# Kernel tuning notes

Hardware: AMD Instinct MI355X
Metric: run time of the kernel (lower is better)

Reference implementation:

```python
import jax, jax.numpy as jnp
import numpy as np

B, S, D = 8, 1024, 256


def _linear_params(key, d):
    k1, k2 = jax.random.split(key)
    lim = 1.0 / np.sqrt(d)
    W = jax.random.uniform(k1, (d, d), jnp.float32, -lim, lim)
    b = jax.random.uniform(k2, (d,), jnp.float32, -lim, lim)
    return W, b


def setup_inputs() -> dict:
    key = jax.random.key(0)
    ks = jax.random.split(key, 7)
    x = jax.random.normal(ks[0], (B, S, D), jnp.float32)
    Wq, bq = _linear_params(ks[1], D)
    Wk, bk = _linear_params(ks[2], D)
    Wv, bv = _linear_params(ks[3], D)
    Wf, bf = _linear_params(ks[4], D)
    Wi, bi = _linear_params(ks[5], D)
    Wo, bo = _linear_params(ks[6], D)
    return {"x": x, "Wq": Wq, "bq": bq, "Wk": Wk, "bk": bk, "Wv": Wv, "bv": bv,
            "Wf": Wf, "bf": bf, "Wi": Wi, "bi": bi, "Wo": Wo, "bo": bo}


def reference(x, Wq, bq, Wk, bk, Wv, bv, Wf, bf, Wi, bi, Wo, bo):
    # Projections (torch Linear stores W as [out, in])
    q = x @ Wq.T + bq
    k = x @ Wk.T + bk
    v = x @ Wq.T + bq  # faithful to source: forward uses self.W_q(x) for v (W_v unused)
    f = jax.nn.sigmoid(x @ Wf.T + bf)  # forget gate, sigmoid
    i = jnp.exp(x @ Wi.T + bi)         # input gate, exp

    # time-major xs: each (S, B, D)
    xs = tuple(jnp.swapaxes(a, 0, 1) for a in (f, i, k, v, q))
    C0 = jnp.zeros((x.shape[0], x.shape[2], x.shape[2]), x.dtype)  # matrix memory [B,D,D]
    n0 = jnp.zeros((x.shape[0], x.shape[2]), x.dtype)              # normalizer [B,D]

    def step(carry, t):
        C, n = carry
        ft, it, kt, vt, qt = t
        # C_t = f_t * C_{t-1} + i_t * v_t k_t^T  (gates broadcast over key dim)
        C = ft[:, :, None] * C + it[:, :, None] * (vt[:, :, None] * kt[:, None, :])
        n = ft * n + it * kt
        num = jnp.einsum('bik,bk->bi', C, qt)
        den = jnp.maximum(jnp.abs(jnp.einsum('bk,bk->b', n, qt)), 1.0)[:, None]
        return (C, n), num / den

    _, h = jax.lax.scan(step, (C0, n0), xs)
    h = jnp.swapaxes(h, 0, 1)  # (B, S, D)
    return h @ Wo.T + bo
```

## Files before the change

### kernel.cpp

```cpp
#include <hip/hip_runtime.h>
#include <math.h>

namespace {

constexpr int Bn = 8;
constexpr int Sn = 1024;
constexpr int Dn = 256;
constexpr int Mn = Bn * Sn;
constexpr int L  = 32;
constexpr int NSEG = Sn / L;

typedef __attribute__((ext_vector_type(8))) short short8;
typedef __attribute__((ext_vector_type(4))) float f32x4;

__device__ float g_den[Bn * Sn];

__device__ __forceinline__ float sigmoidf_(float x) {
    return 1.0f / (1.0f + __expf(-x));
}

__device__ __forceinline__ unsigned short f2bf(float x) {
    unsigned int u = __float_as_uint(x);
    return (unsigned short)((u + 0x7FFF + ((u >> 16) & 1)) >> 16);
}
__device__ __forceinline__ float bf2f(unsigned short h) {
    return __uint_as_float(((unsigned int)h) << 16);
}

__global__ __launch_bounds__(256) void split_xw(
    const float* __restrict__ X,
    const float* __restrict__ Wq, const float* __restrict__ Wk,
    const float* __restrict__ Wf, const float* __restrict__ Wi,
    unsigned short* __restrict__ Xh, unsigned short* __restrict__ Xl,
    unsigned short* __restrict__ Wh, unsigned short* __restrict__ Wl)
{
    const int i = blockIdx.x * 256 + threadIdx.x;
    const float4* src;
    unsigned short* dh;
    unsigned short* dl;
    size_t off;
    if (i < 524288) {
        src = (const float4*)X + i;
        dh = Xh; dl = Xl;
        off = (size_t)i * 4;
    } else {
        const int j = i - 524288;
        const int w = j >> 14;
        const int r = j & 16383;
        const float* Wp = (w == 0) ? Wq : (w == 1) ? Wk : (w == 2) ? Wf : Wi;
        src = (const float4*)Wp + r;
        dh = Wh; dl = Wl;
        off = ((size_t)w << 16) + (size_t)r * 4;
    }
    const float4 v = *src;
    ushort4 h, l;
    h.x = f2bf(v.x); l.x = f2bf(v.x - bf2f(h.x));
    h.y = f2bf(v.y); l.y = f2bf(v.y - bf2f(h.y));
    h.z = f2bf(v.z); l.z = f2bf(v.z - bf2f(h.z));
    h.w = f2bf(v.w); l.w = f2bf(v.w - bf2f(h.w));
    *(ushort4*)(dh + off) = h;
    *(ushort4*)(dl + off) = l;
}

__global__ __launch_bounds__(256) void split_pn(
    const float* __restrict__ Pn, const float* __restrict__ Wo,
    unsigned short* __restrict__ Ph, unsigned short* __restrict__ Pl,
    unsigned short* __restrict__ Woh, unsigned short* __restrict__ Wol)
{
    const int i = blockIdx.x * 256 + threadIdx.x;
    float4 v;
    unsigned short* dh;
    unsigned short* dl;
    size_t off;
    if (i < 524288) {
        const float invd = 1.0f / fmaxf(fabsf(g_den[i >> 6]), 1.0f);
        v = ((const float4*)Pn)[i];
        v.x *= invd; v.y *= invd; v.z *= invd; v.w *= invd;
        dh = Ph; dl = Pl;
        off = (size_t)i * 4;
    } else {
        const int j = i - 524288;
        v = ((const float4*)Wo)[j];
        dh = Woh; dl = Wol;
        off = (size_t)j * 4;
    }
    ushort4 h, l;
    h.x = f2bf(v.x); l.x = f2bf(v.x - bf2f(h.x));
    h.y = f2bf(v.y); l.y = f2bf(v.y - bf2f(h.y));
    h.z = f2bf(v.z); l.z = f2bf(v.z - bf2f(h.z));
    h.w = f2bf(v.w); l.w = f2bf(v.w - bf2f(h.w));
    *(ushort4*)(dh + off) = h;
    *(ushort4*)(dl + off) = l;
}

__global__ __launch_bounds__(256) void proj_gemm2(
    const unsigned short* __restrict__ Xh, const unsigned short* __restrict__ Xl,
    const unsigned short* __restrict__ Wh, const unsigned short* __restrict__ Wl,
    const float* __restrict__ b0, const float* __restrict__ b1,
    const float* __restrict__ b2, const float* __restrict__ b3,
    float* __restrict__ Y0, float* __restrict__ Y1,
    float* __restrict__ Y2, float* __restrict__ Y3)
{
    __shared__ unsigned short Ahs[128][40];
    __shared__ unsigned short Als[128][40];
    __shared__ unsigned short Bhs[128][40];
    __shared__ unsigned short Bls[128][40];

    const int tid = threadIdx.x;
    const int mb  = blockIdx.x * 128;
    const int nbg = blockIdx.y;
    const int widx = nbg >> 1;
    const int ro   = (nbg & 1) * 128;

    const float* bsel = (widx == 0) ? b0 : (widx == 1) ? b1 : (widx == 2) ? b2 : b3;
    float*       Ysel = (widx == 0) ? Y0 : (widx == 1) ? Y1 : (widx == 2) ? Y2 : Y3;

    const int lane = tid & 63;
    const int wv   = tid >> 6;
    const int wm   = (wv >> 1) * 64;
    const int wn   = (wv & 1) * 64;
    const int quad = lane >> 4;
    const int l16  = lane & 15;
    const int srow = tid >> 1;
    const int skq  = (tid & 1) * 16;

    const size_t abase = (size_t)(mb + srow) * Dn + skq;
    const size_t bbase = (size_t)(nbg * 128 + srow) * Dn + skq;

    f32x4 acc[4][4];
    #pragma unroll
    for (int mt = 0; mt < 4; ++mt)
        #pragma unroll
        for (int nt = 0; nt < 4; ++nt)
            acc[mt][nt] = (f32x4){0.f, 0.f, 0.f, 0.f};

    short8 pah0, pah1, pal0, pal1, pbh0, pbh1, pbl0, pbl1;
    pah0 = *(const short8*)(Xh + abase);     pah1 = *(const short8*)(Xh + abase + 8);
    pal0 = *(const short8*)(Xl + abase);     pal1 = *(const short8*)(Xl + abase + 8);
    pbh0 = *(const short8*)(Wh + bbase);     pbh1 = *(const short8*)(Wh + bbase + 8);
    pbl0 = *(const short8*)(Wl + bbase);     pbl1 = *(const short8*)(Wl + bbase + 8);

    for (int k0 = 0; k0 < Dn; k0 += 32) {
        __syncthreads();
        *(short8*)&Ahs[srow][skq]     = pah0;
        *(short8*)&Ahs[srow][skq + 8] = pah1;
        *(short8*)&Als[srow][skq]     = pal0;
        *(short8*)&Als[srow][skq + 8] = pal1;
        *(short8*)&Bhs[srow][skq]     = pbh0;
        *(short8*)&Bhs[srow][skq + 8] = pbh1;
        *(short8*)&Bls[srow][skq]     = pbl0;
        *(short8*)&Bls[srow][skq + 8] = pbl1;
        __syncthreads();

        if (k0 + 32 < Dn) {
            const size_t ka = abase + k0 + 32;
            const size_t kb = bbase + k0 + 32;
            pah0 = *(const short8*)(Xh + ka); pah1 = *(const short8*)(Xh + ka + 8);
            pal0 = *(const short8*)(Xl + ka); pal1 = *(const short8*)(Xl + ka + 8);
            pbh0 = *(const short8*)(Wh + kb); pbh1 = *(const short8*)(Wh + kb + 8);
            pbl0 = *(const short8*)(Wl + kb); pbl1 = *(const short8*)(Wl + kb + 8);
        }

        short8 afh[4], afl[4];
        #pragma unroll
        for (int mt = 0; mt < 4; ++mt) {
            const int row = wm + mt * 16 + l16;
            afh[mt] = *(const short8*)&Ahs[row][quad * 8];
            afl[mt] = *(const short8*)&Als[row][quad * 8];
        }
        #pragma unroll
        for (int nt = 0; nt < 4; ++nt) {
            const int row = wn + nt * 16 + l16;
            const short8 bfh = *(const short8*)&Bhs[row][quad * 8];
            const short8 bfl = *(const short8*)&Bls[row][quad * 8];
            #pragma unroll
            for (int mt = 0; mt < 4; ++mt) {
                acc[mt][nt] = __builtin_amdgcn_mfma_f32_16x16x32_bf16(
                    afh[mt], bfh, acc[mt][nt], 0, 0, 0);
                acc[mt][nt] = __builtin_amdgcn_mfma_f32_16x16x32_bf16(
                    afh[mt], bfl, acc[mt][nt], 0, 0, 0);
                acc[mt][nt] = __builtin_amdgcn_mfma_f32_16x16x32_bf16(
                    afl[mt], bfh, acc[mt][nt], 0, 0, 0);
            }
        }
    }

    #pragma unroll
    for (int nt = 0; nt < 4; ++nt) {
        const int col = ro + wn + nt * 16 + l16;
        const float bv = bsel[col];
        #pragma unroll
        for (int mt = 0; mt < 4; ++mt) {
            const int rowb = mb + wm + mt * 16 + quad * 4;
            #pragma unroll
            for (int r = 0; r < 4; ++r) {
                float v = acc[mt][nt][r] + bv;
                if (widx == 2)      v = sigmoidf_(v);
                else if (widx == 3) v = __expf(v);
                Ysel[(size_t)(rowb + r) * Dn + col] = v;
            }
        }
    }
}

__global__ __launch_bounds__(256) void out_gemm2(
    const unsigned short* __restrict__ Ph, const unsigned short* __restrict__ Pl,
    const unsigned short* __restrict__ Woh, const unsigned short* __restrict__ Wol,
    const float* __restrict__ bias, float* __restrict__ Y)
{
    __shared__ unsigned short Ahs[64][40];
    __shared__ unsigned short Als[64][40];
    __shared__ unsigned short Bhs[64][40];
    __shared__ unsigned short Bls[64][40];

    const int tid = threadIdx.x;
    const int mb  = blockIdx.x * 64;
    const int nb  = blockIdx.y * 64;

    const int lane = tid & 63;
    const int wv   = tid >> 6;
    const int wm   = (wv >> 1) * 32;
    const int wn   = (wv & 1) * 32;
    const int quad = lane >> 4;
    const int l16  = lane & 15;
    const int srow = tid >> 2;
    const int skq  = (tid & 3) * 8;

    const size_t abase = (size_t)(mb + srow) * Dn + skq;
    const size_t bbase = (size_t)(nb + srow) * Dn + skq;

    f32x4 acc[2][2];
    #pragma unroll
    for (int mt = 0; mt < 2; ++mt)
        #pragma unroll
        for (int nt = 0; nt < 2; ++nt)
            acc[mt][nt] = (f32x4){0.f, 0.f, 0.f, 0.f};

    short8 pah, pal, pbh, pbl;
    pah = *(const short8*)(Ph  + abase);
    pal = *(const short8*)(Pl  + abase);
    pbh = *(const short8*)(Woh + bbase);
    pbl = *(const short8*)(Wol + bbase);

    for (int k0 = 0; k0 < Dn; k0 += 32) {
        __syncthreads();
        *(short8*)&Ahs[srow][skq] = pah;
        *(short8*)&Als[srow][skq] = pal;
        *(short8*)&Bhs[srow][skq] = pbh;
        *(short8*)&Bls[srow][skq] = pbl;
        __syncthreads();

        if (k0 + 32 < Dn) {
            const size_t ka = abase + k0 + 32;
            const size_t kb = bbase + k0 + 32;
            pah = *(const short8*)(Ph  + ka);
            pal = *(const short8*)(Pl  + ka);
            pbh = *(const short8*)(Woh + kb);
            pbl = *(const short8*)(Wol + kb);
        }

        short8 afh[2], afl[2];
        #pragma unroll
        for (int mt = 0; mt < 2; ++mt) {
            const int row = wm + mt * 16 + l16;
            afh[mt] = *(const short8*)&Ahs[row][quad * 8];
            afl[mt] = *(const short8*)&Als[row][quad * 8];
        }
        #pragma unroll
        for (int nt = 0; nt < 2; ++nt) {
            const int row = wn + nt * 16 + l16;
            const short8 bfh = *(const short8*)&Bhs[row][quad * 8];
            const short8 bfl = *(const short8*)&Bls[row][quad * 8];
            #pragma unroll
            for (int mt = 0; mt < 2; ++mt) {
                acc[mt][nt] = __builtin_amdgcn_mfma_f32_16x16x32_bf16(
                    afh[mt], bfh, acc[mt][nt], 0, 0, 0);
                acc[mt][nt] = __builtin_amdgcn_mfma_f32_16x16x32_bf16(
                    afh[mt], bfl, acc[mt][nt], 0, 0, 0);
                acc[mt][nt] = __builtin_amdgcn_mfma_f32_16x16x32_bf16(
                    afl[mt], bfh, acc[mt][nt], 0, 0, 0);
            }
        }
    }

    #pragma unroll
    for (int nt = 0; nt < 2; ++nt) {
        const int col = nb + wn + nt * 16 + l16;
        const float bv = bias[col];
        #pragma unroll
        for (int mt = 0; mt < 2; ++mt) {
            const int rowb = mb + wm + mt * 16 + quad * 4;
            #pragma unroll
            for (int r = 0; r < 4; ++r) {
                Y[(size_t)(rowb + r) * Dn + col] = acc[mt][nt][r] + bv;
            }
        }
    }
}

__global__ __launch_bounds__(256) void prep(
    const float* __restrict__ Pf, const float* __restrict__ Pi,
    const float* __restrict__ Pk, const float* __restrict__ Pq,
    float* __restrict__ Gc, float* __restrict__ Vt, float* __restrict__ Nt,
    float* __restrict__ Aend, float* __restrict__ un, float* __restrict__ Ssm)
{
    const int m = blockIdx.x;
    const int b = blockIdx.y;
    const int tid = threadIdx.x;

    if (tid < L) g_den[b * Sn + m * L + tid] = 0.0f;

    {
        const int r = tid;
        const size_t base = (size_t)b * Sn * Dn + (size_t)m * L * Dn + r;
        float G = 1.0f, Nacc = 0.0f;
        #pragma unroll 4
        for (int t = 0; t < L; ++t) {
            const size_t off = base + (size_t)t * Dn;
            const float f  = Pf[off];
            const float iv = Pi[off];
            const float kv = Pk[off];
            const float vv = Pq[off];
            G *= f;
            const float rG = 1.0f / G;
            Gc[off] = G;
            Vt[off] = iv * vv * rG;
            Nacc = fmaf(iv * kv, rG, Nacc);
            Nt[off] = Nacc;
        }
        const size_t s = ((size_t)b * NSEG + m) * Dn + r;
        Aend[s] = G;
        un[s]   = G * Nacc;
    }

    {
        const size_t qb = (size_t)b * Sn * Dn + (size_t)m * L * Dn;
        const int tau = tid >> 3;
        const int s4  = (tid & 7) * 4;

        float a0 = 0.f, a1 = 0.f, a2 = 0.f, a3 = 0.f;
        #pragma unroll 4
        for (int c = 0; c < Dn; c += 4) {
            const float4 q4 = *(const float4*)(Pq + qb + (size_t)tau * Dn + c);
            const float4 k0 = *(const float4*)(Pk + qb + (size_t)(s4 + 0) * Dn + c);
            const float4 k1 = *(const float4*)(Pk + qb + (size_t)(s4 + 1) * Dn + c);
            const float4 k2 = *(const float4*)(Pk + qb + (size_t)(s4 + 2) * Dn + c);
            const float4 k3 = *(const float4*)(Pk + qb + (size_t)(s4 + 3) * Dn + c);
            a0 += q4.x*k0.x + q4.y*k0.y + q4.z*k0.z + q4.w*k0.w;
            a1 += q4.x*k1.x + q4.y*k1.y + q4.z*k1.z + q4.w*k1.w;
            a2 += q4.x*k2.x + q4.y*k2.y + q4.z*k2.z + q4.w*k2.w;
            a3 += q4.x*k3.x + q4.y*k3.y + q4.z*k3.z + q4.w*k3.w;
        }
        float* outp = Ssm + ((size_t)b * NSEG + m) * L * L + (size_t)tau * L + s4;
        outp[0] = (s4 + 0 <= tau) ? a0 : 0.0f;
        outp[1] = (s4 + 1 <= tau) ? a1 : 0.0f;
        outp[2] = (s4 + 2 <= tau) ? a2 : 0.0f;
        outp[3] = (s4 + 3 <= tau) ? a3 : 0.0f;
    }
}

__global__ __launch_bounds__(256) void ut_gemm(
    const float* __restrict__ Pk, const float* __restrict__ Vt,
    const float* __restrict__ Aend, float* __restrict__ UT)
{
    __shared__ float As[L][68];
    __shared__ float Bs[L][68];

    const int bm   = blockIdx.x;
    const int tile = blockIdx.y;
    const int cb   = (tile >> 2) * 64;
    const int rb   = (tile & 3) * 64;
    const int b    = bm >> 5;
    const int m    = bm & 31;
    const size_t kb = (size_t)b * Sn * Dn + (size_t)m * L * Dn;
    const int tid = threadIdx.x;

    #pragma unroll
    for (int n = 0; n < 8; ++n) {
        const int e  = n * 256 + tid;
        const int sg = e >> 6;
        const int cc = e & 63;
        As[sg][cc] = Pk[kb + (size_t)sg * Dn + cb + cc];
        Bs[sg][cc] = Vt[kb + (size_t)sg * Dn + rb + cc];
    }
    __syncthreads();

    const int tx = tid & 15;
    const int ty = tid >> 4;
    float acc[4][4];
    #pragma unroll
    for (int i = 0; i < 4; ++i)
        #pragma unroll
        for (int j = 0; j < 4; ++j) acc[i][j] = 0.0f;

    #pragma unroll
    for (int sg = 0; sg < L; ++sg) {
        const float4 a4 = *(const float4*)&As[sg][ty * 4];
        const float4 b4 = *(const float4*)&Bs[sg][tx * 4];
        const float aa[4] = {a4.x, a4.y, a4.z, a4.w};
        const float bb[4] = {b4.x, b4.y, b4.z, b4.w};
        #pragma unroll
        for (int i = 0; i < 4; ++i)
            #pragma unroll
            for (int j = 0; j < 4; ++j)
                acc[i][j] = fmaf(aa[i], bb[j], acc[i][j]);
    }

    const float4 g4 = *(const float4*)(Aend + (size_t)bm * Dn + rb + tx * 4);
    float* ub = UT + (size_t)bm * Dn * Dn;
    #pragma unroll
    for (int i = 0; i < 4; ++i) {
        float4 o;
        o.x = acc[i][0] * g4.x; o.y = acc[i][1] * g4.y;
        o.z = acc[i][2] * g4.z; o.w = acc[i][3] * g4.w;
        *(float4*)(ub + (size_t)(cb + ty * 4 + i) * Dn + rb + tx * 4) = o;
    }
}

__global__ __launch_bounds__(256) void compose(
    const float* __restrict__ UT, const float* __restrict__ Aend,
    const float* __restrict__ un,
    float* __restrict__ CinT, float* __restrict__ nin)
{
    const int gx = blockIdx.x;
    const int b  = blockIdx.y;
    const int tid = threadIdx.x;

    if (gx == 64) {
        const int r = tid;
        float acc = 0.0f;
        for (int m = 0; m < NSEG; ++m) {
            const size_t s = ((size_t)b * NSEG + m) * Dn + r;
            nin[s] = acc;
            acc = fmaf(Aend[s], acc, un[s]);
        }
        return;
    }

    const int id = gx * 256 + tid;
    const int c  = id >> 6;
    const int r4 = (id & 63) * 4;

    float4 acc = make_float4(0.f, 0.f, 0.f, 0.f);
    for (int m = 0; m < NSEG; ++m) {
        const size_t bm  = (size_t)b * NSEG + m;
        const size_t idx = bm * Dn * Dn + (size_t)c * Dn + r4;
        *(float4*)(CinT + idx) = acc;
        const float4 a4 = *(const float4*)(Aend + bm * Dn + r4);
        const float4 u4 = *(const float4*)(UT + idx);
        acc.x = fmaf(a4.x, acc.x, u4.x);
        acc.y = fmaf(a4.y, acc.y, u4.y);
        acc.z = fmaf(a4.z, acc.z, u4.z);
        acc.w = fmaf(a4.w, acc.w, u4.w);
    }
}

__global__ __launch_bounds__(256) void num_gemm(
    const float* __restrict__ Pq, const float* __restrict__ Vt,
    const float* __restrict__ Gc, const float* __restrict__ Ssm,
    const float* __restrict__ CinT, const float* __restrict__ Nt,
    const float* __restrict__ nin, float* __restrict__ Pnum)
{
    __shared__ float Sld[L][33];
    __shared__ float Qld[L][257];

    const int rb = blockIdx.x * 128;
    const int m  = blockIdx.y;
    const int b  = blockIdx.z;
    const size_t qb = (size_t)b * Sn * Dn + (size_t)m * L * Dn;
    const size_t ub = ((size_t)b * NSEG + m) * Dn * Dn;
    const size_t sb = ((size_t)b * NSEG + m) * L * L;
    const int tid = threadIdx.x;

    #pragma unroll
    for (int n = 0; n < 4; ++n) {
        const int e = n * 256 + tid;
        Sld[e >> 5][e & 31] = Ssm[sb + e];
    }
    #pragma unroll
    for (int n = 0; n < L; ++n)
        Qld[n][tid] = Pq[qb + (size_t)n * Dn + tid];
    __syncthreads();

    const int tx = tid & 31;
    const int ty = tid >> 5;
    const int r4 = rb + tx * 4;
    const int t4 = ty * 4;

    float4 acc[4];
    #pragma unroll
    for (int i = 0; i < 4; ++i) acc[i] = make_float4(0.f, 0.f, 0.f, 0.f);

    #pragma unroll 4
    for (int sg = 0; sg < L; ++sg) {
        const float4 v4 = *(const float4*)(Vt + qb + (size_t)sg * Dn + r4);
        #pragma unroll
        for (int i = 0; i < 4; ++i) {
            const float s = Sld[t4 + i][sg];
            acc[i].x = fmaf(s, v4.x, acc[i].x);
            acc[i].y = fmaf(s, v4.y, acc[i].y);
            acc[i].z = fmaf(s, v4.z, acc[i].z);
            acc[i].w = fmaf(s, v4.w, acc[i].w);
        }
    }

    #pragma unroll 8
    for (int c = 0; c < Dn; ++c) {
        const float4 ct = *(const float4*)(CinT + ub + (size_t)c * Dn + r4);
        #pragma unroll
        for (int i = 0; i < 4; ++i) {
            const float q = Qld[t4 + i][c];
            acc[i].x = fmaf(q, ct.x, acc[i].x);
            acc[i].y = fmaf(q, ct.y, acc[i].y);
            acc[i].z = fmaf(q, ct.z, acc[i].z);
            acc[i].w = fmaf(q, ct.w, acc[i].w);
        }
    }

    const float4 i4 = *(const float4*)(nin + ((size_t)b * NSEG + m) * Dn + r4);
    float dp[4];
    #pragma unroll
    for (int i = 0; i < 4; ++i) {
        const size_t off = qb + (size_t)(t4 + i) * Dn + r4;
        const float4 g4 = *(const float4*)(Gc + off);
        const float4 q4 = *(const float4*)(Pq + off);
        const float4 n4 = *(const float4*)(Nt + off);
        float4 o;
        o.x = acc[i].x * g4.x; o.y = acc[i].y * g4.y;
        o.z = acc[i].z * g4.z; o.w = acc[i].w * g4.w;
        *(float4*)(Pnum + off) = o;
        dp[i] = q4.x * g4.x * (i4.x + n4.x)
              + q4.y * g4.y * (i4.y + n4.y)
              + q4.z * g4.z * (i4.z + n4.z)
              + q4.w * g4.w * (i4.w + n4.w);
    }

    #pragma unroll
    for (int s = 1; s < 32; s <<= 1) {
        #pragma unroll
        for (int i = 0; i < 4; ++i)
            dp[i] += __shfl_xor(dp[i], s, 64);
    }
    if (tx == 0) {
        #pragma unroll
        for (int i = 0; i < 4; ++i)
            atomicAdd(&g_den[b * Sn + m * L + t4 + i], dp[i]);
    }
}

}

extern "C" void kernel_launch(void* const* d_in, const int* in_sizes, int n_in,
                              void* d_out, int out_size, void* d_ws, size_t ws_size,
                              hipStream_t stream)
{
    const float* x  = (const float*)d_in[0];
    const float* Wq = (const float*)d_in[1];  const float* bq = (const float*)d_in[2];
    const float* Wk = (const float*)d_in[3];  const float* bk = (const float*)d_in[4];
    const float* Wf = (const float*)d_in[7];  const float* bf = (const float*)d_in[8];
    const float* Wi = (const float*)d_in[9];  const float* bi = (const float*)d_in[10];
    const float* Wo = (const float*)d_in[11]; const float* bo = (const float*)d_in[12];
    float* out = (float*)d_out;

    float* ws = (float*)d_ws;
    const size_t sz = (size_t)Mn * Dn;
    float* Pq = ws;
    float* Pk = ws + sz;
    float* Pf = ws + 2 * sz;
    float* Pi = ws + 3 * sz;
    float* Pn = ws + 4 * sz;
    float* Gc = ws + 5 * sz;
    float* Vt = ws + 6 * sz;
    float* Nt = ws + 7 * sz;
    float* UT   = ws + 8 * sz;
    float* CinT = ws + 16 * sz;
    float* Ssm  = ws + 24 * sz;
    float* Aend = Ssm + (size_t)Bn * NSEG * L * L;
    float* un   = Aend + (size_t)Bn * NSEG * Dn;
    float* nin  = un   + (size_t)Bn * NSEG * Dn;

    unsigned short* Xh = (unsigned short*)UT;
    unsigned short* Xl = Xh + sz;
    unsigned short* Wh = Xl + sz;
    unsigned short* Wl = Wh + (size_t)1024 * Dn;
    unsigned short* Ph  = (unsigned short*)UT;
    unsigned short* Pl  = Ph + sz;
    unsigned short* Woh = (unsigned short*)Ssm;
    unsigned short* Wol = Woh + (size_t)Dn * Dn;

    split_xw<<<dim3(2304), 256, 0, stream>>>(x, Wq, Wk, Wf, Wi, Xh, Xl, Wh, Wl);

    proj_gemm2<<<dim3(Mn / 128, 8), 256, 0, stream>>>(
        Xh, Xl, Wh, Wl, bq, bk, bf, bi, Pq, Pk, Pf, Pi);

    prep<<<dim3(NSEG, Bn), 256, 0, stream>>>(
        Pf, Pi, Pk, Pq, Gc, Vt, Nt, Aend, un, Ssm);

    ut_gemm<<<dim3(Bn * NSEG, 16), 256, 0, stream>>>(Pk, Vt, Aend, UT);

    compose<<<dim3(65, Bn), 256, 0, stream>>>(UT, Aend, un, CinT, nin);

    num_gemm<<<dim3(2, NSEG, Bn), 256, 0, stream>>>(
        Pq, Vt, Gc, Ssm, CinT, Nt, nin, Pn);

    split_pn<<<dim3(2112), 256, 0, stream>>>(Pn, Wo, Ph, Pl, Woh, Wol);

    out_gemm2<<<dim3(Mn / 64, Dn / 64), 256, 0, stream>>>(
        Ph, Pl, Woh, Wol, bo, out);
}
```

Measured before the change: 227.7 us.

## Stage K/Q chunk in LDS and run scan and QK^T on separate thread halves

The prep kernel now launches 512 threads and first loads the segment's K and Q tiles (32x256 each) into padded shared memory. The first 256 threads run the per-channel gate cumulative scan while the other 256 compute the masked intra-chunk QK^T matrix concurrently. The scan also batches its forget and input gate loads eight timesteps ahead. This removes repeated global reads of K and Q in the dot-product loop and overlaps the two phases that previously ran one after the other. In exchange it uses about 66KB of LDS per block, which limits occupancy, and changes the key-row interleave in the QK^T stage.

```diff
diff --git a/kernel.cpp b/kernel.cpp
--- a/kernel.cpp
+++ b/kernel.cpp
@@ -298,64 +298,89 @@
     }
 }
 
-__global__ __launch_bounds__(256) void prep(
+__global__ __launch_bounds__(512) void prep(
     const float* __restrict__ Pf, const float* __restrict__ Pi,
     const float* __restrict__ Pk, const float* __restrict__ Pq,
     float* __restrict__ Gc, float* __restrict__ Vt, float* __restrict__ Nt,
     float* __restrict__ Aend, float* __restrict__ un, float* __restrict__ Ssm)
 {
+    __shared__ float Ks[L][260];
+    __shared__ float Qs[L][260];
+
     const int m = blockIdx.x;
     const int b = blockIdx.y;
     const int tid = threadIdx.x;
+    const size_t qb = (size_t)b * Sn * Dn + (size_t)m * L * Dn;
 
     if (tid < L) g_den[b * Sn + m * L + tid] = 0.0f;
 
-    {
+    #pragma unroll
+    for (int p = 0; p < 4; ++p) {
+        const int lin = p * 512 + tid;
+        const int row = lin >> 6;
+        const int c4  = (lin & 63) * 4;
+        *(float4*)&Ks[row][c4] = *(const float4*)(Pk + qb + (size_t)row * Dn + c4);
+    }
+    #pragma unroll
+    for (int p = 0; p < 4; ++p) {
+        const int lin = p * 512 + tid;
+        const int row = lin >> 6;
+        const int c4  = (lin & 63) * 4;
+        *(float4*)&Qs[row][c4] = *(const float4*)(Pq + qb + (size_t)row * Dn + c4);
+    }
+    __syncthreads();
+
+    if (tid < 256) {
         const int r = tid;
-        const size_t base = (size_t)b * Sn * Dn + (size_t)m * L * Dn + r;
+        const size_t base = qb + r;
         float G = 1.0f, Nacc = 0.0f;
-        #pragma unroll 4
-        for (int t = 0; t < L; ++t) {
-            const size_t off = base + (size_t)t * Dn;
-            const float f  = Pf[off];
-            const float iv = Pi[off];
-            const float kv = Pk[off];
-            const float vv = Pq[off];
-            G *= f;
-            const float rG = 1.0f / G;
-            Gc[off] = G;
-            Vt[off] = iv * vv * rG;
-            Nacc = fmaf(iv * kv, rG, Nacc);
-            Nt[off] = Nacc;
+        for (int tb = 0; tb < L; tb += 8) {
+            float fv[8], iv[8];
+            #pragma unroll
+            for (int u = 0; u < 8; ++u) {
+                fv[u] = Pf[base + (size_t)(tb + u) * Dn];
+                iv[u] = Pi[base + (size_t)(tb + u) * Dn];
+            }
+            #pragma unroll
+            for (int u = 0; u < 8; ++u) {
+                const int t = tb + u;
+                const size_t off = base + (size_t)t * Dn;
+                const float kv = Ks[t][r];
+                const float vv = Qs[t][r];
+                G *= fv[u];
+                const float rG = 1.0f / G;
+                Gc[off] = G;
+                Vt[off] = iv[u] * vv * rG;
+                Nacc = fmaf(iv[u] * kv, rG, Nacc);
+                Nt[off] = Nacc;
+            }
         }
         const size_t s = ((size_t)b * NSEG + m) * Dn + r;
         Aend[s] = G;
         un[s]   = G * Nacc;
-    }
-
-    {
-        const size_t qb = (size_t)b * Sn * Dn + (size_t)m * L * Dn;
-        const int tau = tid >> 3;
-        const int s4  = (tid & 7) * 4;
+    } else {
+        const int t2  = tid - 256;
+        const int tau = t2 >> 3;
+        const int sb0 = t2 & 7;
 
         float a0 = 0.f, a1 = 0.f, a2 = 0.f, a3 = 0.f;
         #pragma unroll 4
         for (int c = 0; c < Dn; c += 4) {
-            const float4 q4 = *(const float4*)(Pq + qb + (size_t)tau * Dn + c);
-            const float4 k0 = *(const float4*)(Pk + qb + (size_t)(s4 + 0) * Dn + c);
-            const float4 k1 = *(const float4*)(Pk + qb + (size_t)(s4 + 1) * Dn + c);
-            const float4 k2 = *(const float4*)(Pk + qb + (size_t)(s4 + 2) * Dn + c);
-            const float4 k3 = *(const float4*)(Pk + qb + (size_t)(s4 + 3) * Dn + c);
+            const float4 q4 = *(const float4*)&Qs[tau][c];
+            const float4 k0 = *(const float4*)&Ks[sb0     ][c];
+            const float4 k1 = *(const float4*)&Ks[sb0 +  8][c];
+            const float4 k2 = *(const float4*)&Ks[sb0 + 16][c];
+            const float4 k3 = *(const float4*)&Ks[sb0 + 24][c];
             a0 += q4.x*k0.x + q4.y*k0.y + q4.z*k0.z + q4.w*k0.w;
             a1 += q4.x*k1.x + q4.y*k1.y + q4.z*k1.z + q4.w*k1.w;
             a2 += q4.x*k2.x + q4.y*k2.y + q4.z*k2.z + q4.w*k2.w;
             a3 += q4.x*k3.x + q4.y*k3.y + q4.z*k3.z + q4.w*k3.w;
         }
-        float* outp = Ssm + ((size_t)b * NSEG + m) * L * L + (size_t)tau * L + s4;
-        outp[0] = (s4 + 0 <= tau) ? a0 : 0.0f;
-        outp[1] = (s4 + 1 <= tau) ? a1 : 0.0f;
-        outp[2] = (s4 + 2 <= tau) ? a2 : 0.0f;
-        outp[3] = (s4 + 3 <= tau) ? a3 : 0.0f;
+        float* outp = Ssm + ((size_t)b * NSEG + m) * L * L + (size_t)tau * L;
+        outp[sb0     ] = (sb0      <= tau) ? a0 : 0.0f;
+        outp[sb0 +  8] = (sb0 +  8 <= tau) ? a1 : 0.0f;
+        outp[sb0 + 16] = (sb0 + 16 <= tau) ? a2 : 0.0f;
+        outp[sb0 + 24] = (sb0 + 24 <= tau) ? a3 : 0.0f;
     }
 }
 
@@ -593,7 +618,7 @@
     proj_gemm2<<<dim3(Mn / 128, 8), 256, 0, stream>>>(
         Xh, Xl, Wh, Wl, bq, bk, bf, bi, Pq, Pk, Pf, Pi);
 
-    prep<<<dim3(NSEG, Bn), 256, 0, stream>>>(
+    prep<<<dim3(NSEG, Bn), 512, 0, stream>>>(
         Pf, Pi, Pk, Pq, Gc, Vt, Nt, Aend, un, Ssm);
 
     ut_gemm<<<dim3(Bn * NSEG, 16), 256, 0, stream>>>(Pk, Vt, Aend, UT);
```

New measurement: 203.1 us. 10.8% less time.
